# Kernel tuning notes

Hardware: AMD Instinct MI355X
Metric: run time of the kernel (lower is better)

## Reference

```python
import jax, jax.numpy as jnp
import numpy as np

DIM = 1024
NUM_HEADS = 16
HEAD_DIM = DIM // NUM_HEADS
SCALE = HEAD_DIM ** (-0.5)


def setup_inputs() -> dict:
    key = jax.random.key(0)
    ks = jax.random.split(key, 5)
    b, n = 4, 1370
    x = jax.random.normal(ks[0], (b, n, DIM), dtype=jnp.float32)
    # Dense kernels: Keras Dense stores kernel as [in, out]
    w_qkv = jax.random.normal(ks[1], (DIM, 3 * DIM), dtype=jnp.float32) * (DIM ** -0.5)
    b_qkv = jnp.zeros((3 * DIM,), dtype=jnp.float32)
    w_proj = jax.random.normal(ks[2], (DIM, DIM), dtype=jnp.float32) * (DIM ** -0.5)
    b_proj = jnp.zeros((DIM,), dtype=jnp.float32)
    return {"x": x, "w_qkv": w_qkv, "b_qkv": b_qkv, "w_proj": w_proj, "b_proj": b_proj}


def reference(x, w_qkv, b_qkv, w_proj, b_proj):
    b, n, _ = x.shape
    qkv = x @ w_qkv + b_qkv                       # [b, n, 3*dim]
    qkv = qkv.reshape(b, n, 3, NUM_HEADS, HEAD_DIM)
    qkv = jnp.transpose(qkv, (2, 0, 3, 1, 4))     # [3, b, h, n, d]
    q, k, v = qkv[0], qkv[1], qkv[2]
    q = q * jnp.asarray(SCALE, dtype=q.dtype)
    attn = jnp.einsum("bhqd,bhkd->bhqk", q, k)    # [b, h, n, n]
    attn = jax.nn.softmax(attn, axis=-1)
    out = jnp.einsum("bhqk,bhkd->bhqd", attn, v)  # [b, h, n, d]
    out = jnp.transpose(out, (0, 2, 1, 3)).reshape(b, n, DIM)
    return out @ w_proj + b_proj
```

## Files before the change

kernel.cpp:

```cpp
#include <hip/hip_runtime.h>
#include <stdint.h>
#include <math.h>

typedef __attribute__((ext_vector_type(8))) __bf16 bf16x8;
typedef __attribute__((ext_vector_type(4))) __bf16 bf16x4;
typedef __attribute__((ext_vector_type(4))) float f32x4;
typedef __attribute__((ext_vector_type(8))) short short8;

#define MFMA(a, b, c) __builtin_amdgcn_mfma_f32_16x16x32_bf16((a), (b), (c), 0, 0, 0)

constexpr int DIMC  = 1024;
constexpr int HEADS = 16;
constexpr int HD    = 64;
constexpr int BATCH = 4;
constexpr int SEQ   = 1370;
constexpr int MROWS = BATCH * SEQ;
constexpr int NPAD  = 1408;
constexpr float QK_SCALE = 0.125f * 1.44269504088896341f;

__device__ __forceinline__ unsigned short f2bf(float f) {
    union { float f; unsigned int u; } v; v.f = f;
    unsigned int r = (v.u + 0x7FFFu + ((v.u >> 16) & 1u)) >> 16;
    return (unsigned short)r;
}

__device__ __forceinline__ void gl2lds16(const unsigned short* g, unsigned short* l) {
    __builtin_amdgcn_global_load_lds(
        (const __attribute__((address_space(1))) unsigned int*)g,
        (__attribute__((address_space(3))) unsigned int*)l,
        16, 0, 0);
}

__global__ void cast_x_kernel(const float* __restrict__ x, unsigned short* __restrict__ xb, int nvec) {
    int i = blockIdx.x * blockDim.x + threadIdx.x;
    if (i >= nvec) return;
    f32x4 a = reinterpret_cast<const f32x4*>(x)[2 * i];
    f32x4 b = reinterpret_cast<const f32x4*>(x)[2 * i + 1];
    short8 o;
    o[0] = (short)f2bf(a[0]); o[1] = (short)f2bf(a[1]);
    o[2] = (short)f2bf(a[2]); o[3] = (short)f2bf(a[3]);
    o[4] = (short)f2bf(b[0]); o[5] = (short)f2bf(b[1]);
    o[6] = (short)f2bf(b[2]); o[7] = (short)f2bf(b[3]);
    reinterpret_cast<short8*>(xb)[i] = o;
}

__global__ __launch_bounds__(256) void transpose_cast_kernel(const float* __restrict__ in,
                                                             unsigned short* __restrict__ out,
                                                             int R, int C) {
    __shared__ float tile[32][33];
    int tx = threadIdx.x & 31, ty = threadIdx.x >> 5;
    int cbase = blockIdx.x * 32, rbase = blockIdx.y * 32;
#pragma unroll
    for (int rr = 0; rr < 4; ++rr) {
        int r = ty + rr * 8;
        tile[r][tx] = in[(size_t)(rbase + r) * C + cbase + tx];
    }
    __syncthreads();
#pragma unroll
    for (int rr = 0; rr < 4; ++rr) {
        int cr = ty + rr * 8;
        out[(size_t)(cbase + cr) * R + rbase + tx] = f2bf(tile[tx][cr]);
    }
}

__global__ void zero_vpad_kernel(unsigned short* __restrict__ vTg) {
    int idx = blockIdx.x * blockDim.x + threadIdx.x;
    const int padw = NPAD - SEQ;
    const int total = 64 * 64 * padw;
    if (idx >= total) return;
    int col = SEQ + idx % padw;
    int rowflat = idx / padw;
    vTg[(size_t)rowflat * NPAD + col] = 0;
}

template <int EPI>
__global__ __launch_bounds__(512) void gemm_bt_kernel(const unsigned short* __restrict__ A,
                                                      const unsigned short* __restrict__ Bt,
                                                      int M, int N, int K, int Nx,
                                                      const float* __restrict__ bias,
                                                      unsigned short* __restrict__ qg,
                                                      unsigned short* __restrict__ kg,
                                                      unsigned short* __restrict__ vTg,
                                                      float* __restrict__ outf) {
    __shared__ unsigned short As[2][128 * 32];
    __shared__ unsigned short Bs[2][128 * 32];
    const int tid = threadIdx.x;
    const int l = tid & 63, w = tid >> 6;
    const int wr = w >> 2, wc = w & 3;
    const int lm = l & 15, lk = l >> 4;

    int nwg = gridDim.x;
    int wgid = (blockIdx.x & 7) * (nwg >> 3) + (blockIdx.x >> 3);
    int bx = wgid % Nx, by = wgid / Nx;
    const int brow = by * 128, bcol = bx * 128;

    f32x4 acc[4][2];
#pragma unroll
    for (int i = 0; i < 4; ++i)
#pragma unroll
        for (int j = 0; j < 2; ++j) acc[i][j] = f32x4{0.f, 0.f, 0.f, 0.f};

    const int srow = tid >> 2;
    const int ssrc = (((tid & 3) ^ ((srow >> 1) & 3)) << 3);
    auto stage = [&](int kt, int buf) {
        int ga = min(brow + srow, M - 1);
        gl2lds16(&A[(size_t)ga * K + kt * 32 + ssrc], &As[buf][tid * 8]);
        int gb = bcol + srow;
        gl2lds16(&Bt[(size_t)gb * K + kt * 32 + ssrc], &Bs[buf][tid * 8]);
    };

    const int nkt = K >> 5;
    stage(0, 0);
    __syncthreads();
    int cur = 0;
    for (int kt = 0; kt < nkt; ++kt) {
        if (kt + 1 < nkt) stage(kt + 1, cur ^ 1);

        const int swa = (lk ^ ((lm >> 1) & 3)) * 8;
        bf16x8 af[4], bfr[2];
#pragma unroll
        for (int i = 0; i < 4; ++i)
            af[i] = *reinterpret_cast<const bf16x8*>(&As[cur][(wr * 64 + i * 16 + lm) * 32 + swa]);
#pragma unroll
        for (int j = 0; j < 2; ++j)
            bfr[j] = *reinterpret_cast<const bf16x8*>(&Bs[cur][(wc * 32 + j * 16 + lm) * 32 + swa]);
        __builtin_amdgcn_s_setprio(1);
#pragma unroll
        for (int i = 0; i < 4; ++i)
#pragma unroll
            for (int j = 0; j < 2; ++j)
                acc[i][j] = MFMA(af[i], bfr[j], acc[i][j]);
        __builtin_amdgcn_s_setprio(0);
        __syncthreads();
        cur ^= 1;
    }

#pragma unroll
    for (int i = 0; i < 4; ++i) {
        int mbase = brow + wr * 64 + i * 16 + lk * 4;
#pragma unroll
        for (int j = 0; j < 2; ++j) {
            int col = bcol + wc * 32 + j * 16 + lm;
            float bv = bias[col];
#pragma unroll
            for (int r = 0; r < 4; ++r) {
                int m = mbase + r;
                if (m >= M) continue;
                float val = acc[i][j][r] + bv;
                if constexpr (EPI == 0) {
                    int which = col >> 10;
                    int head = (col >> 6) & 15;
                    int d = col & 63;
                    int b = m / SEQ;
                    int nseq = m - b * SEQ;
                    int bh = b * HEADS + head;
                    if (which == 0) {
                        qg[((size_t)bh * SEQ + nseq) * HD + d] = f2bf(val * QK_SCALE);
                    } else if (which == 1) {
                        kg[((size_t)bh * SEQ + nseq) * HD + d] = f2bf(val);
                    } else {
                        vTg[((size_t)bh * HD + d) * NPAD + nseq] = f2bf(val);
                    }
                } else {
                    outf[(size_t)m * DIMC + col] = val;
                }
            }
        }
    }
}

__global__ __launch_bounds__(512) void attn_kernel(const unsigned short* __restrict__ qg,
                                                   const unsigned short* __restrict__ kg,
                                                   const unsigned short* __restrict__ vTg,
                                                   unsigned short* __restrict__ ao) {
    __shared__ unsigned short Ks[64 * 72];
    __shared__ unsigned short Vs[64 * 72];
    __shared__ unsigned short Pw[8][16 * 72];

    const int tid = threadIdx.x;
    const int l = tid & 63, w = tid >> 6;
    const int lm = l & 15, lk = l >> 4;

    int wg = (blockIdx.x & 7) * 88 + (blockIdx.x >> 3);
    const int bh = wg / 11;
    const int qbase = (wg - bh * 11) * 128;

    int qr = min(qbase + w * 16 + lm, SEQ - 1);
    const unsigned short* qp = &qg[((size_t)bh * SEQ + qr) * HD + lk * 8];
    bf16x8 qf0 = *reinterpret_cast<const bf16x8*>(qp);
    bf16x8 qf1 = *reinterpret_cast<const bf16x8*>(qp + 32);

    f32x4 o[4];
#pragma unroll
    for (int jd = 0; jd < 4; ++jd) o[jd] = f32x4{0.f, 0.f, 0.f, 0.f};
    float mrun = -INFINITY, lrun = 0.f;

    const int r0 = tid >> 3;
    const int c8b = (tid & 7) << 3;
    const unsigned short* kbase = &kg[(size_t)bh * SEQ * HD];
    const unsigned short* vbase = &vTg[(size_t)bh * HD * NPAD];

    short8 kr, vr;
    auto load_tile = [&](int t) {
        int kvg = min(t * 64 + r0, SEQ - 1);
        kr = *reinterpret_cast<const short8*>(&kbase[(size_t)kvg * HD + c8b]);
        vr = *reinterpret_cast<const short8*>(&vbase[(size_t)r0 * NPAD + t * 64 + c8b]);
    };
    auto write_tile = [&]() {
        *reinterpret_cast<short8*>(&Ks[r0 * 72 + c8b]) = kr;
        *reinterpret_cast<short8*>(&Vs[r0 * 72 + c8b]) = vr;
    };

    const int NT = (SEQ + 63) >> 6;
    load_tile(0);
    for (int t = 0; t < NT; ++t) {
        write_tile();
        __syncthreads();
        if (t + 1 < NT) load_tile(t + 1);

        f32x4 s[4];
        __builtin_amdgcn_s_setprio(1);
#pragma unroll
        for (int j = 0; j < 4; ++j) {
            f32x4 z = {0.f, 0.f, 0.f, 0.f};
            bf16x8 k0 = *reinterpret_cast<const bf16x8*>(&Ks[(j * 16 + lm) * 72 + lk * 8]);
            bf16x8 k1 = *reinterpret_cast<const bf16x8*>(&Ks[(j * 16 + lm) * 72 + 32 + lk * 8]);
            z = MFMA(k0, qf0, z);
            z = MFMA(k1, qf1, z);
            s[j] = z;
        }
        __builtin_amdgcn_s_setprio(0);

        if (t == NT - 1) {
#pragma unroll
            for (int j = 0; j < 4; ++j)
#pragma unroll
                for (int r = 0; r < 4; ++r) {
                    int kvg = t * 64 + j * 16 + lk * 4 + r;
                    if (kvg >= SEQ) s[j][r] = -INFINITY;
                }
        }

        float tmax = s[0][0];
#pragma unroll
        for (int j = 0; j < 4; ++j)
#pragma unroll
            for (int r = 0; r < 4; ++r) tmax = fmaxf(tmax, s[j][r]);

        if (!__all(tmax - mrun <= 8.0f)) {
            float tm = fmaxf(tmax, __shfl_xor(tmax, 16));
            tm = fmaxf(tm, __shfl_xor(tm, 32));
            float mnew = fmaxf(mrun, tm);
            float scale = exp2f(mrun - mnew);
            mrun = mnew;
            lrun *= scale;
            float sc[4];
#pragma unroll
            for (int r = 0; r < 4; ++r) sc[r] = __shfl(scale, lk * 4 + r);
#pragma unroll
            for (int jd = 0; jd < 4; ++jd) {
                o[jd][0] *= sc[0]; o[jd][1] *= sc[1];
                o[jd][2] *= sc[2]; o[jd][3] *= sc[3];
            }
        }

        float p[4][4];
        float psum = 0.f;
#pragma unroll
        for (int j = 0; j < 4; ++j)
#pragma unroll
            for (int r = 0; r < 4; ++r) {
                float pv = exp2f(s[j][r] - mrun);
                p[j][r] = pv;
                psum += pv;
            }
        lrun += psum;

#pragma unroll
        for (int j = 0; j < 4; ++j) {
            bf16x4 pk;
            pk[0] = (__bf16)p[j][0]; pk[1] = (__bf16)p[j][1];
            pk[2] = (__bf16)p[j][2]; pk[3] = (__bf16)p[j][3];
            *reinterpret_cast<bf16x4*>(&Pw[w][lm * 72 + j * 16 + lk * 4]) = pk;
        }

        bf16x8 pa0 = *reinterpret_cast<const bf16x8*>(&Pw[w][lm * 72 + lk * 8]);
        bf16x8 pa1 = *reinterpret_cast<const bf16x8*>(&Pw[w][lm * 72 + 32 + lk * 8]);
        __builtin_amdgcn_s_setprio(1);
#pragma unroll
        for (int jd = 0; jd < 4; ++jd) {
            bf16x8 v0 = *reinterpret_cast<const bf16x8*>(&Vs[(jd * 16 + lm) * 72 + lk * 8]);
            bf16x8 v1 = *reinterpret_cast<const bf16x8*>(&Vs[(jd * 16 + lm) * 72 + 32 + lk * 8]);
            o[jd] = MFMA(pa0, v0, o[jd]);
            o[jd] = MFMA(pa1, v1, o[jd]);
        }
        __builtin_amdgcn_s_setprio(0);
        __syncthreads();
    }

    float ltot = lrun;
    ltot += __shfl_xor(ltot, 16);
    ltot += __shfl_xor(ltot, 32);
    float linv = 1.f / ltot;
    int b = bh >> 4, h = bh & 15;
#pragma unroll
    for (int r = 0; r < 4; ++r) {
        int q = qbase + w * 16 + lk * 4 + r;
        float inv = __shfl(linv, lk * 4 + r);
        if (q >= SEQ) continue;
#pragma unroll
        for (int jd = 0; jd < 4; ++jd) {
            ao[((size_t)b * SEQ + q) * DIMC + h * HD + jd * 16 + lm] = f2bf(o[jd][r] * inv);
        }
    }
}

extern "C" void kernel_launch(void* const* d_in, const int* in_sizes, int n_in,
                              void* d_out, int out_size, void* d_ws, size_t ws_size,
                              hipStream_t stream) {
    const float* x      = (const float*)d_in[0];
    const float* w_qkv  = (const float*)d_in[1];
    const float* b_qkv  = (const float*)d_in[2];
    const float* w_proj = (const float*)d_in[3];
    const float* b_proj = (const float*)d_in[4];
    float* out = (float*)d_out;

    char* ws = (char*)d_ws;
    unsigned short* xb     = (unsigned short*)ws; ws += (size_t)MROWS * DIMC * 2;
    unsigned short* wqkvT  = (unsigned short*)ws; ws += (size_t)3 * DIMC * DIMC * 2;
    unsigned short* wprojT = (unsigned short*)ws; ws += (size_t)DIMC * DIMC * 2;
    unsigned short* qg     = (unsigned short*)ws; ws += (size_t)64 * SEQ * HD * 2;
    unsigned short* kg     = (unsigned short*)ws; ws += (size_t)64 * SEQ * HD * 2;
    unsigned short* vTg    = (unsigned short*)ws; ws += (size_t)64 * HD * NPAD * 2;
    unsigned short* ao     = (unsigned short*)ws; ws += (size_t)MROWS * DIMC * 2;

    const int nvec = MROWS * DIMC / 8;
    cast_x_kernel<<<(nvec + 255) / 256, 256, 0, stream>>>(x, xb, nvec);
    transpose_cast_kernel<<<dim3(3 * DIMC / 32, DIMC / 32), 256, 0, stream>>>(w_qkv, wqkvT, DIMC, 3 * DIMC);
    transpose_cast_kernel<<<dim3(DIMC / 32, DIMC / 32), 256, 0, stream>>>(w_proj, wprojT, DIMC, DIMC);
    zero_vpad_kernel<<<(64 * 64 * (NPAD - SEQ) + 255) / 256, 256, 0, stream>>>(vTg);

    gemm_bt_kernel<0><<<dim3(24 * 43), 512, 0, stream>>>(
        xb, wqkvT, MROWS, 3 * DIMC, DIMC, 24, b_qkv, qg, kg, vTg, nullptr);

    attn_kernel<<<dim3(8 * 88), 512, 0, stream>>>(qg, kg, vTg, ao);

    gemm_bt_kernel<1><<<dim3(8 * 43), 512, 0, stream>>>(
        ao, wprojT, MROWS, DIMC, DIMC, 8, b_proj, nullptr, nullptr, nullptr, out);
}
```

Baseline: 178.8 us.

## Fuse fp32-to-bf16 cast of x into QKV GEMM A-tile staging

Drops the separate cast_x kernel and has the QKV GEMM read x directly as fp32 through registers. It converts to bf16 and writes the swizzled LDS tile after the MFMAs, so the global load overlaps compute. This saves one launch and a full write and read of the bf16 copy of x, but the A operand now costs twice the global bytes per tile and adds VGPR pressure. The block-to-tile mapping is also changed so that each XCD gets a stripe of column tiles, aimed at better L2 reuse of B.

```diff
diff --git a/kernel.cpp b/kernel.cpp
--- a/kernel.cpp
+++ b/kernel.cpp
@@ -31,19 +31,6 @@
         16, 0, 0);
 }
 
-__global__ void cast_x_kernel(const float* __restrict__ x, unsigned short* __restrict__ xb, int nvec) {
-    int i = blockIdx.x * blockDim.x + threadIdx.x;
-    if (i >= nvec) return;
-    f32x4 a = reinterpret_cast<const f32x4*>(x)[2 * i];
-    f32x4 b = reinterpret_cast<const f32x4*>(x)[2 * i + 1];
-    short8 o;
-    o[0] = (short)f2bf(a[0]); o[1] = (short)f2bf(a[1]);
-    o[2] = (short)f2bf(a[2]); o[3] = (short)f2bf(a[3]);
-    o[4] = (short)f2bf(b[0]); o[5] = (short)f2bf(b[1]);
-    o[6] = (short)f2bf(b[2]); o[7] = (short)f2bf(b[3]);
-    reinterpret_cast<short8*>(xb)[i] = o;
-}
-
 __global__ __launch_bounds__(256) void transpose_cast_kernel(const float* __restrict__ in,
                                                              unsigned short* __restrict__ out,
                                                              int R, int C) {
@@ -74,7 +61,8 @@
 }
 
 template <int EPI>
-__global__ __launch_bounds__(512) void gemm_bt_kernel(const unsigned short* __restrict__ A,
+__global__ __launch_bounds__(512) void gemm_bt_kernel(const float* __restrict__ Ax,
+                                                      const unsigned short* __restrict__ Ab,
                                                       const unsigned short* __restrict__ Bt,
                                                       int M, int N, int K, int Nx,
                                                       const float* __restrict__ bias,
@@ -89,9 +77,10 @@
     const int wr = w >> 2, wc = w & 3;
     const int lm = l & 15, lk = l >> 4;
 
-    int nwg = gridDim.x;
-    int wgid = (blockIdx.x & 7) * (nwg >> 3) + (blockIdx.x >> 3);
-    int bx = wgid % Nx, by = wgid / Nx;
+    const int stripe = Nx >> 3;
+    int xcd = blockIdx.x & 7, bi = blockIdx.x >> 3;
+    int bx = xcd * stripe + bi % stripe;
+    int by = bi / stripe;
     const int brow = by * 128, bcol = bx * 128;
 
     f32x4 acc[4][2];
@@ -101,20 +90,50 @@
         for (int j = 0; j < 2; ++j) acc[i][j] = f32x4{0.f, 0.f, 0.f, 0.f};
 
     const int srow = tid >> 2;
-    const int ssrc = (((tid & 3) ^ ((srow >> 1) & 3)) << 3);
-    auto stage = [&](int kt, int buf) {
-        int ga = min(brow + srow, M - 1);
-        gl2lds16(&A[(size_t)ga * K + kt * 32 + ssrc], &As[buf][tid * 8]);
-        int gb = bcol + srow;
+    const int kc = tid & 3;
+    const int ssrc = ((kc ^ ((srow >> 1) & 3)) << 3);
+    const int ga = min(brow + srow, M - 1);
+    const int gb = bcol + srow;
+
+    auto stageB = [&](int kt, int buf) {
         gl2lds16(&Bt[(size_t)gb * K + kt * 32 + ssrc], &Bs[buf][tid * 8]);
     };
+    auto stageA_lds = [&](int kt, int buf) {
+        gl2lds16(&Ab[(size_t)ga * K + kt * 32 + ssrc], &As[buf][tid * 8]);
+    };
+    auto loadA_f32 = [&](int kt, f32x4& a0, f32x4& a1) {
+        const float* p = &Ax[(size_t)ga * K + kt * 32 + kc * 8];
+        a0 = *reinterpret_cast<const f32x4*>(p);
+        a1 = *reinterpret_cast<const f32x4*>(p + 4);
+    };
+    auto writeA_f32 = [&](int buf, const f32x4& a0, const f32x4& a1) {
+        short8 o;
+        o[0] = (short)f2bf(a0[0]); o[1] = (short)f2bf(a0[1]);
+        o[2] = (short)f2bf(a0[2]); o[3] = (short)f2bf(a0[3]);
+        o[4] = (short)f2bf(a1[0]); o[5] = (short)f2bf(a1[1]);
+        o[6] = (short)f2bf(a1[2]); o[7] = (short)f2bf(a1[3]);
+        *reinterpret_cast<short8*>(&As[buf][srow * 32 + ((kc ^ ((srow >> 1) & 3)) << 3)]) = o;
+    };
 
     const int nkt = K >> 5;
-    stage(0, 0);
+    f32x4 pa0, pa1;
+    if constexpr (EPI == 0) {
+        loadA_f32(0, pa0, pa1);
+        stageB(0, 0);
+        writeA_f32(0, pa0, pa1);
+    } else {
+        stageA_lds(0, 0);
+        stageB(0, 0);
+    }
     __syncthreads();
+
     int cur = 0;
     for (int kt = 0; kt < nkt; ++kt) {
-        if (kt + 1 < nkt) stage(kt + 1, cur ^ 1);
+        if (kt + 1 < nkt) {
+            if constexpr (EPI == 0) loadA_f32(kt + 1, pa0, pa1);
+            else stageA_lds(kt + 1, cur ^ 1);
+            stageB(kt + 1, cur ^ 1);
+        }
 
         const int swa = (lk ^ ((lm >> 1) & 3)) * 8;
         bf16x8 af[4], bfr[2];
@@ -131,6 +150,10 @@
             for (int j = 0; j < 2; ++j)
                 acc[i][j] = MFMA(af[i], bfr[j], acc[i][j]);
         __builtin_amdgcn_s_setprio(0);
+
+        if constexpr (EPI == 0) {
+            if (kt + 1 < nkt) writeA_f32(cur ^ 1, pa0, pa1);
+        }
         __syncthreads();
         cur ^= 1;
     }
@@ -326,7 +349,6 @@
     float* out = (float*)d_out;
 
     char* ws = (char*)d_ws;
-    unsigned short* xb     = (unsigned short*)ws; ws += (size_t)MROWS * DIMC * 2;
     unsigned short* wqkvT  = (unsigned short*)ws; ws += (size_t)3 * DIMC * DIMC * 2;
     unsigned short* wprojT = (unsigned short*)ws; ws += (size_t)DIMC * DIMC * 2;
     unsigned short* qg     = (unsigned short*)ws; ws += (size_t)64 * SEQ * HD * 2;
@@ -334,17 +356,15 @@
     unsigned short* vTg    = (unsigned short*)ws; ws += (size_t)64 * HD * NPAD * 2;
     unsigned short* ao     = (unsigned short*)ws; ws += (size_t)MROWS * DIMC * 2;
 
-    const int nvec = MROWS * DIMC / 8;
-    cast_x_kernel<<<(nvec + 255) / 256, 256, 0, stream>>>(x, xb, nvec);
     transpose_cast_kernel<<<dim3(3 * DIMC / 32, DIMC / 32), 256, 0, stream>>>(w_qkv, wqkvT, DIMC, 3 * DIMC);
     transpose_cast_kernel<<<dim3(DIMC / 32, DIMC / 32), 256, 0, stream>>>(w_proj, wprojT, DIMC, DIMC);
     zero_vpad_kernel<<<(64 * 64 * (NPAD - SEQ) + 255) / 256, 256, 0, stream>>>(vTg);
 
     gemm_bt_kernel<0><<<dim3(24 * 43), 512, 0, stream>>>(
-        xb, wqkvT, MROWS, 3 * DIMC, DIMC, 24, b_qkv, qg, kg, vTg, nullptr);
+        x, nullptr, wqkvT, MROWS, 3 * DIMC, DIMC, 24, b_qkv, qg, kg, vTg, nullptr);
 
     attn_kernel<<<dim3(8 * 88), 512, 0, stream>>>(qg, kg, vTg, ao);
 
     gemm_bt_kernel<1><<<dim3(8 * 43), 512, 0, stream>>>(
-        ao, wprojT, MROWS, DIMC, DIMC, 8, b_proj, nullptr, nullptr, nullptr, out);
-}
+        nullptr, ao, wprojT, MROWS, DIMC, DIMC, 8, b_proj, nullptr, nullptr, nullptr, out);
+}
```

Result: slower. 196.0 us (+9.7%).

## Use 256x256x64 tiles with deeper async pipelining for the QKV GEMM

Applied to the files above, without the earlier changes.

Splits the shared GEMM into a dedicated QKV kernel and a projection kernel. The QKV kernel moves from 128x128x32 to 256x256x64 tiles with a 128 KB double buffer, an XOR swizzle over 8 chunks, and a partial vmcnt wait so the next tile's loads overlap the MFMAs, which raises arithmetic intensity and cuts global traffic. The grid drops to 264 blocks (22 row tiles x 12 column tiles), which risks poor wave balance on the CU count, plus higher register pressure from 32 accumulators per lane. The projection kernel gets only minor hoisting of its row indices.

```diff
diff --git a/kernel.cpp b/kernel.cpp
--- a/kernel.cpp
+++ b/kernel.cpp
@@ -73,15 +73,135 @@
     vTg[(size_t)rowflat * NPAD + col] = 0;
 }
 
-template <int EPI>
-__global__ __launch_bounds__(512) void gemm_bt_kernel(const unsigned short* __restrict__ A,
-                                                      const unsigned short* __restrict__ Bt,
-                                                      int M, int N, int K, int Nx,
-                                                      const float* __restrict__ bias,
-                                                      unsigned short* __restrict__ qg,
-                                                      unsigned short* __restrict__ kg,
-                                                      unsigned short* __restrict__ vTg,
-                                                      float* __restrict__ outf) {
+__global__ __launch_bounds__(512, 2) void gemm_qkv_kernel(const unsigned short* __restrict__ A,
+                                                          const unsigned short* __restrict__ Bt,
+                                                          int M, int N, int K, int Nx,
+                                                          const float* __restrict__ bias,
+                                                          unsigned short* __restrict__ qg,
+                                                          unsigned short* __restrict__ kg,
+                                                          unsigned short* __restrict__ vTg) {
+    __shared__ unsigned short As[2][256 * 64];
+    __shared__ unsigned short Bs[2][256 * 64];
+    const int tid = threadIdx.x;
+    const int l = tid & 63, w = tid >> 6;
+    const int wr = w >> 2, wc = w & 3;
+    const int lm = l & 15, lk = l >> 4;
+
+    int nwg = gridDim.x;
+    int wgid = (blockIdx.x & 7) * (nwg >> 3) + (blockIdx.x >> 3);
+    int bx = wgid % Nx, by = wgid / Nx;
+    const int brow = by * 256, bcol = bx * 256;
+
+    f32x4 acc[8][4];
+#pragma unroll
+    for (int i = 0; i < 8; ++i)
+#pragma unroll
+        for (int j = 0; j < 4; ++j) acc[i][j] = f32x4{0.f, 0.f, 0.f, 0.f};
+
+    auto stage = [&](int kt, int buf) {
+#pragma unroll
+        for (int Lq = 0; Lq < 4; ++Lq) {
+            int cid = Lq * 512 + tid;
+            int row = cid >> 3, kc = cid & 7;
+            int src = ((kc ^ (row & 7)) << 3);
+            int ga = min(brow + row, M - 1);
+            gl2lds16(&A[(size_t)ga * K + kt * 64 + src], &As[buf][cid * 8]);
+        }
+#pragma unroll
+        for (int Lq = 0; Lq < 4; ++Lq) {
+            int cid = Lq * 512 + tid;
+            int row = cid >> 3, kc = cid & 7;
+            int src = ((kc ^ (row & 7)) << 3);
+            int gb = bcol + row;
+            gl2lds16(&Bt[(size_t)gb * K + kt * 64 + src], &Bs[buf][cid * 8]);
+        }
+    };
+
+    const int nkt = K >> 6;
+    stage(0, 0);
+    int cur = 0;
+    for (int kt = 0; kt < nkt; ++kt) {
+        if (kt + 1 < nkt) {
+            stage(kt + 1, cur ^ 1);
+            asm volatile("s_waitcnt vmcnt(8)" ::: "memory");
+        } else {
+            asm volatile("s_waitcnt vmcnt(0)" ::: "memory");
+        }
+        __builtin_amdgcn_s_barrier();
+
+#pragma unroll
+        for (int mh = 0; mh < 2; ++mh) {
+            bf16x8 af[4][2];
+#pragma unroll
+            for (int m4 = 0; m4 < 4; ++m4)
+#pragma unroll
+                for (int ks = 0; ks < 2; ++ks) {
+                    int row = wr * 128 + (mh * 4 + m4) * 16 + lm;
+                    int slot = (ks * 4 + lk) ^ (lm & 7);
+                    af[m4][ks] = *reinterpret_cast<const bf16x8*>(&As[cur][row * 64 + slot * 8]);
+                }
+#pragma unroll
+            for (int nh = 0; nh < 2; ++nh) {
+                bf16x8 bfr[2][2];
+#pragma unroll
+                for (int n2 = 0; n2 < 2; ++n2)
+#pragma unroll
+                    for (int ks = 0; ks < 2; ++ks) {
+                        int row = wc * 64 + (nh * 2 + n2) * 16 + lm;
+                        int slot = (ks * 4 + lk) ^ (lm & 7);
+                        bfr[n2][ks] = *reinterpret_cast<const bf16x8*>(&Bs[cur][row * 64 + slot * 8]);
+                    }
+                __builtin_amdgcn_s_setprio(1);
+#pragma unroll
+                for (int m4 = 0; m4 < 4; ++m4)
+#pragma unroll
+                    for (int n2 = 0; n2 < 2; ++n2)
+#pragma unroll
+                        for (int ks = 0; ks < 2; ++ks)
+                            acc[mh * 4 + m4][nh * 2 + n2] =
+                                MFMA(af[m4][ks], bfr[n2][ks], acc[mh * 4 + m4][nh * 2 + n2]);
+                __builtin_amdgcn_s_setprio(0);
+            }
+        }
+        __builtin_amdgcn_s_barrier();
+        cur ^= 1;
+    }
+
+#pragma unroll
+    for (int i = 0; i < 8; ++i) {
+        int mbase = brow + wr * 128 + i * 16 + lk * 4;
+#pragma unroll
+        for (int j = 0; j < 4; ++j) {
+            int col = bcol + wc * 64 + j * 16 + lm;
+            float bv = bias[col];
+            int which = col >> 10;
+            int head = (col >> 6) & 15;
+            int d = col & 63;
+#pragma unroll
+            for (int r = 0; r < 4; ++r) {
+                int m = mbase + r;
+                if (m >= M) continue;
+                float val = acc[i][j][r] + bv;
+                int b = m / SEQ;
+                int nseq = m - b * SEQ;
+                int bh = b * HEADS + head;
+                if (which == 0) {
+                    qg[((size_t)bh * SEQ + nseq) * HD + d] = f2bf(val * QK_SCALE);
+                } else if (which == 1) {
+                    kg[((size_t)bh * SEQ + nseq) * HD + d] = f2bf(val);
+                } else {
+                    vTg[((size_t)bh * HD + d) * NPAD + nseq] = f2bf(val);
+                }
+            }
+        }
+    }
+}
+
+__global__ __launch_bounds__(512) void gemm_proj_kernel(const unsigned short* __restrict__ A,
+                                                        const unsigned short* __restrict__ Bt,
+                                                        int M, int N, int K, int Nx,
+                                                        const float* __restrict__ bias,
+                                                        float* __restrict__ outf) {
     __shared__ unsigned short As[2][128 * 32];
     __shared__ unsigned short Bs[2][128 * 32];
     const int tid = threadIdx.x;
@@ -102,10 +222,10 @@
 
     const int srow = tid >> 2;
     const int ssrc = (((tid & 3) ^ ((srow >> 1) & 3)) << 3);
+    const int ga = min(brow + srow, M - 1);
+    const int gb = bcol + srow;
     auto stage = [&](int kt, int buf) {
-        int ga = min(brow + srow, M - 1);
         gl2lds16(&A[(size_t)ga * K + kt * 32 + ssrc], &As[buf][tid * 8]);
-        int gb = bcol + srow;
         gl2lds16(&Bt[(size_t)gb * K + kt * 32 + ssrc], &Bs[buf][tid * 8]);
     };
 
@@ -146,24 +266,7 @@
             for (int r = 0; r < 4; ++r) {
                 int m = mbase + r;
                 if (m >= M) continue;
-                float val = acc[i][j][r] + bv;
-                if constexpr (EPI == 0) {
-                    int which = col >> 10;
-                    int head = (col >> 6) & 15;
-                    int d = col & 63;
-                    int b = m / SEQ;
-                    int nseq = m - b * SEQ;
-                    int bh = b * HEADS + head;
-                    if (which == 0) {
-                        qg[((size_t)bh * SEQ + nseq) * HD + d] = f2bf(val * QK_SCALE);
-                    } else if (which == 1) {
-                        kg[((size_t)bh * SEQ + nseq) * HD + d] = f2bf(val);
-                    } else {
-                        vTg[((size_t)bh * HD + d) * NPAD + nseq] = f2bf(val);
-                    }
-                } else {
-                    outf[(size_t)m * DIMC + col] = val;
-                }
+                outf[(size_t)m * DIMC + col] = acc[i][j][r] + bv;
             }
         }
     }
@@ -340,11 +443,11 @@
     transpose_cast_kernel<<<dim3(DIMC / 32, DIMC / 32), 256, 0, stream>>>(w_proj, wprojT, DIMC, DIMC);
     zero_vpad_kernel<<<(64 * 64 * (NPAD - SEQ) + 255) / 256, 256, 0, stream>>>(vTg);
 
-    gemm_bt_kernel<0><<<dim3(24 * 43), 512, 0, stream>>>(
-        xb, wqkvT, MROWS, 3 * DIMC, DIMC, 24, b_qkv, qg, kg, vTg, nullptr);
+    gemm_qkv_kernel<<<dim3(264), 512, 0, stream>>>(
+        xb, wqkvT, MROWS, 3 * DIMC, DIMC, 12, b_qkv, qg, kg, vTg);
 
     attn_kernel<<<dim3(8 * 88), 512, 0, stream>>>(qg, kg, vTg, ao);
 
-    gemm_bt_kernel<1><<<dim3(8 * 43), 512, 0, stream>>>(
-        ao, wprojT, MROWS, DIMC, DIMC, 8, b_proj, nullptr, nullptr, nullptr, out);
-}
+    gemm_proj_kernel<<<dim3(8 * 43), 512, 0, stream>>>(
+        ao, wprojT, MROWS, DIMC, DIMC, 8, b_proj, out);
+}
```

Measured after the change: 223.4 us. 1.25x slower.
